# Kernel tuning notes

Measured on AMD Instinct MI355X. Metric: run time of the kernel, lower is better.

Reference implementation:

```python
import jax, jax.numpy as jnp
import numpy as np

N_NODES = 100000
N_EDGES = 400000
N_GRAPHS = 1000
DIM = 5
N_OUT = 2
EPS = 1e-5


def _linear_params(key, fan_in, fan_out):
    kw, kb = jax.random.split(key)
    s = 1.0 / np.sqrt(fan_in)
    w = jax.random.uniform(kw, (fan_in, fan_out), minval=-s, maxval=s, dtype=jnp.float32)
    b = jax.random.uniform(kb, (fan_out,), minval=-s, maxval=s, dtype=jnp.float32)
    return w, b


def _gn_params(c):
    # rows: [weight, bias, mean_scale] as in PyG GraphNorm init (1, 0, 1)
    return jnp.stack([jnp.ones((c,)), jnp.zeros((c,)), jnp.ones((c,))], axis=0).astype(jnp.float32)


def setup_inputs() -> dict:
    key = jax.random.key(0)
    ks = jax.random.split(key, 16)
    x = jax.random.normal(ks[0], (N_NODES, DIM), dtype=jnp.float32)
    edge_index = jax.random.randint(ks[1], (2, N_EDGES), 0, N_NODES, dtype=jnp.int64)
    batch = jnp.sort(jax.random.randint(ks[2], (N_NODES,), 0, N_GRAPHS, dtype=jnp.int64))
    c1_w1, c1_b1 = _linear_params(ks[3], 2 * DIM, 128)
    c1_w2, c1_b2 = _linear_params(ks[4], 128, 128)
    c1_w3, c1_b3 = _linear_params(ks[5], 128, 128)
    c2_w1, c2_b1 = _linear_params(ks[6], 2 * 128, 256)
    c2_w2, c2_b2 = _linear_params(ks[7], 256, 256)
    c3_w1, c3_b1 = _linear_params(ks[8], 2 * 256, 256)
    lin_w1, lin_b1 = _linear_params(ks[9], 256, 256)
    lin_w2, lin_b2 = _linear_params(ks[10], 256, N_OUT)
    return {
        "x": x, "edge_index": edge_index, "batch": batch,
        "c1_w1": c1_w1, "c1_b1": c1_b1, "c1_gn1": _gn_params(128),
        "c1_w2": c1_w2, "c1_b2": c1_b2, "c1_gn2": _gn_params(128),
        "c1_w3": c1_w3, "c1_b3": c1_b3, "c1_gn3": _gn_params(128),
        "c2_w1": c2_w1, "c2_b1": c2_b1, "c2_gn1": _gn_params(256),
        "c2_w2": c2_w2, "c2_b2": c2_b2, "c2_gn2": _gn_params(256),
        "c3_w1": c3_w1, "c3_b1": c3_b1, "c3_gn1": _gn_params(256),
        "lin_w1": lin_w1, "lin_b1": lin_b1, "lin_w2": lin_w2, "lin_b2": lin_b2,
    }


def _graph_norm(h, p):
    # PyG GraphNorm with batch=None: normalize over all rows (single graph)
    g, b, ms = p[0], p[1], p[2]
    m = h.mean(axis=0)
    out = h - ms * m
    var = (out * out).mean(axis=0)
    return g * out * jax.lax.rsqrt(var + EPS) + b


def _edge_conv(x, src, dst, layers):
    # EdgeConv message: nn(cat[x_i, x_j - x_i]) aggregated (mean) at target i
    xi = x[dst]                                     # [E, C]
    h = jnp.concatenate([xi, x[src] - xi], axis=-1)  # [E, 2C]
    for w, b, gp in layers:
        h = jax.nn.relu(_graph_norm(h @ w + b, gp))
    s = jax.ops.segment_sum(h, dst, num_segments=N_NODES)
    ones = jnp.ones((dst.shape[0], 1), dtype=h.dtype)
    cnt = jax.ops.segment_sum(ones, dst, num_segments=N_NODES)
    return s / jnp.maximum(cnt, 1.0)


def reference(x, edge_index, batch,
              c1_w1, c1_b1, c1_gn1, c1_w2, c1_b2, c1_gn2, c1_w3, c1_b3, c1_gn3,
              c2_w1, c2_b1, c2_gn1, c2_w2, c2_b2, c2_gn2,
              c3_w1, c3_b1, c3_gn1,
              lin_w1, lin_b1, lin_w2, lin_b2):
    src, dst = edge_index[0], edge_index[1]
    h = _edge_conv(x, src, dst, [(c1_w1, c1_b1, c1_gn1), (c1_w2, c1_b2, c1_gn2), (c1_w3, c1_b3, c1_gn3)])
    h = _edge_conv(h, src, dst, [(c2_w1, c2_b1, c2_gn1), (c2_w2, c2_b2, c2_gn2)])
    h = _edge_conv(h, src, dst, [(c3_w1, c3_b1, c3_gn1)])
    # global_mean_pool over graphs (dropout = identity in eval)
    gs = jax.ops.segment_sum(h, batch, num_segments=N_GRAPHS)
    gc = jax.ops.segment_sum(jnp.ones((h.shape[0], 1), h.dtype), batch, num_segments=N_GRAPHS)
    g = gs / jnp.maximum(gc, 1.0)                   # [G, 256]
    out = jax.nn.relu(g @ lin_w1 + lin_b1) @ lin_w2 + lin_b2  # [G, n_out]
    return out
```

## Files before the change

### kernel.cpp

```cpp
#include <hip/hip_runtime.h>
#include <hip/hip_bf16.h>

#define NN 100000
#define NE 400000
#define NG 1000

typedef __attribute__((ext_vector_type(8))) short bf16x8;
typedef __attribute__((ext_vector_type(4))) float f32x4;

__device__ __forceinline__ float bf2f(unsigned short h) {
    return __uint_as_float((unsigned)h << 16);
}
__device__ __forceinline__ unsigned short f2bf(float f) {
    unsigned u = __float_as_uint(f);
    return (unsigned short)((u + 0x7FFFu + ((u >> 16) & 1u)) >> 16);
}
__device__ __forceinline__ void up8(uint4 u, float v[8]) {
    v[0] = bf2f((unsigned short)u.x); v[1] = bf2f((unsigned short)(u.x >> 16));
    v[2] = bf2f((unsigned short)u.y); v[3] = bf2f((unsigned short)(u.y >> 16));
    v[4] = bf2f((unsigned short)u.z); v[5] = bf2f((unsigned short)(u.z >> 16));
    v[6] = bf2f((unsigned short)u.w); v[7] = bf2f((unsigned short)(u.w >> 16));
}
__device__ __forceinline__ uint4 pk8(const float v[8]) {
    uint4 r;
    r.x = (uint)f2bf(v[0]) | ((uint)f2bf(v[1]) << 16);
    r.y = (uint)f2bf(v[2]) | ((uint)f2bf(v[3]) << 16);
    r.z = (uint)f2bf(v[4]) | ((uint)f2bf(v[5]) << 16);
    r.w = (uint)f2bf(v[6]) | ((uint)f2bf(v[7]) << 16);
    return r;
}

__global__ void diag_kernel(float* __restrict__ out, int n, float val) {
    int i = blockIdx.x * 256 + threadIdx.x;
    if (i < n) out[i] = val;
}

__global__ void deg_kernel(const int* __restrict__ dst, int* __restrict__ deg) {
    int e = blockIdx.x * 256 + threadIdx.x;
    if (e < NE) atomicAdd(&deg[dst[e]], 1);
}

__global__ void invdeg_kernel(const int* __restrict__ deg, float* __restrict__ invdeg) {
    int n = blockIdx.x * 256 + threadIdx.x;
    if (n < NN) invdeg[n] = 1.0f / (float)(deg[n] > 0 ? deg[n] : 1);
}

__global__ void scan1_kernel(const int* __restrict__ deg, int* __restrict__ off,
                             int* __restrict__ bsum) {
    __shared__ int s[1024];
    int tid = threadIdx.x;
    int i = blockIdx.x * 1024 + tid;
    int v = (i < NN) ? deg[i] : 0;
    s[tid] = v;
    __syncthreads();
    for (int d = 1; d < 1024; d <<= 1) {
        int add = (tid >= d) ? s[tid - d] : 0;
        __syncthreads();
        s[tid] += add;
        __syncthreads();
    }
    if (i < NN) off[i] = s[tid] - v;
    if (tid == 1023) bsum[blockIdx.x] = s[1023];
}

__global__ void scan2_kernel(int* __restrict__ bsum, int nb) {
    __shared__ int s[128];
    int tid = threadIdx.x;
    int v = (tid < nb) ? bsum[tid] : 0;
    s[tid] = v;
    __syncthreads();
    for (int d = 1; d < 128; d <<= 1) {
        int add = (tid >= d) ? s[tid - d] : 0;
        __syncthreads();
        s[tid] += add;
        __syncthreads();
    }
    if (tid < nb) bsum[tid] = s[tid] - v;
}

__global__ void scan3_kernel(int* __restrict__ off, const int* __restrict__ bsum,
                             int* __restrict__ cursor) {
    int i = blockIdx.x * 256 + threadIdx.x;
    if (i < NN) {
        int o = off[i] + bsum[i >> 10];
        off[i] = o;
        cursor[i] = o;
    }
    if (i == 0) off[NN] = NE;
}

__global__ void sortedge_kernel(const int* __restrict__ src, const int* __restrict__ dst,
                                int* __restrict__ cursor, int* __restrict__ ssrc,
                                int* __restrict__ sdst) {
    int e = blockIdx.x * 256 + threadIdx.x;
    if (e < NE) {
        int d = dst[e];
        int pos = atomicAdd(&cursor[d], 1);
        ssrc[pos] = src[e];
        sdst[pos] = d;
    }
}

__global__ void conv1_node_kernel(const float* __restrict__ x, const float* __restrict__ W,
                                  unsigned short* __restrict__ RQ) {
    __shared__ float Ws[1280];
    for (int i = threadIdx.x; i < 1280; i += 256) Ws[i] = W[i];
    __syncthreads();
    int c = threadIdx.x & 127;
    int which = threadIdx.x >> 7;
    for (int n = blockIdx.x; n < NN; n += gridDim.x) {
        float acc = 0.f;
        #pragma unroll
        for (int r = 0; r < 5; r++) {
            float xv = x[n * 5 + r];
            float bot = Ws[(5 + r) * 128 + c];
            float w = which ? bot : (Ws[r * 128 + c] - bot);
            acc = fmaf(xv, w, acc);
        }
        RQ[(size_t)n * 256 + threadIdx.x] = f2bf(acc);
    }
}

__global__ void wtrans_kernel(const float* __restrict__ W, unsigned short* __restrict__ Wt,
                              int K, int N) {
    int idx = blockIdx.x * 256 + threadIdx.x;
    if (idx >= K * N) return;
    int c = idx / K, k = idx - c * K;
    Wt[(size_t)c * K + k] = f2bf(W[(size_t)k * N + c]);
}

__global__ void wprime_t_kernel(const float* __restrict__ W, unsigned short* __restrict__ Wpt,
                                int K, int C) {
    int idx = blockIdx.x * 256 + threadIdx.x;
    if (idx >= 2 * C * K) return;
    int n = idx / K, k = idx - n * K;
    float v;
    if (n < C) v = W[(size_t)k * C + n] - W[(size_t)(K + k) * C + n];
    else       v = W[(size_t)(K + k) * C + (n - C)];
    Wpt[(size_t)n * K + k] = f2bf(v);
}

template<int C>
__global__ void gstats_node_kernel(const unsigned short* __restrict__ RQ,
                                   const int* __restrict__ ssrc, const int* __restrict__ off,
                                   const float* __restrict__ bias,
                                   float* __restrict__ ssum, float* __restrict__ ssq) {
    constexpr int GPB = 256 / C;
    const int t = threadIdx.x;
    const int c = t % C, g = t / C;
    float b = bias[c];
    float ls = 0.f, lq = 0.f;
    int chunk = (NN + gridDim.x - 1) / gridDim.x;
    int nb = blockIdx.x * chunk, ne = min(nb + chunk, NN);
    for (int n = nb + g; n < ne; n += GPB) {
        float R = bf2f(RQ[(size_t)n * (2 * C) + c]);
        int e0 = off[n], e1 = off[n + 1];
        for (int e = e0; e < e1; e++) {
            float v = R + bf2f(RQ[(size_t)ssrc[e] * (2 * C) + C + c]) + b;
            ls += v; lq += v * v;
        }
    }
    __shared__ float red[2][256];
    red[0][t] = ls; red[1][t] = lq;
    __syncthreads();
    if (t < C) {
        float s = 0.f, q = 0.f;
        #pragma unroll
        for (int gg = 0; gg < GPB; gg++) { s += red[0][gg * C + t]; q += red[1][gg * C + t]; }
        atomicAdd(&ssum[t], s);
        atomicAdd(&ssq[t], q);
    }
}

__global__ void finalize_kernel(const float* __restrict__ ssum, const float* __restrict__ ssq,
                                const float* __restrict__ gn, int C, float invM,
                                float* __restrict__ alpha, float* __restrict__ beta) {
    int c = threadIdx.x;
    if (c >= C) return;
    float g = gn[c], b = gn[C + c], ms = gn[2 * C + c];
    float m = ssum[c] * invM;
    float var = ssq[c] * invM - m * m * ms * (2.f - ms);
    float inv = rsqrtf(var + 1e-5f);
    alpha[c] = g * inv;
    beta[c] = b - g * inv * ms * m;
}

template<int TK, int BN, bool GATHER, bool NORMRELU, bool ROWSC, bool STATS, bool STORE,
         bool SCAT, bool AF32>
__global__ __launch_bounds__(256) void mgemm_kernel(
    const void* __restrict__ Av, const int* __restrict__ gsrc, const int* __restrict__ gdst,
    const float* __restrict__ biasIn, const unsigned short* __restrict__ Wt,
    const float* __restrict__ alpha, const float* __restrict__ beta,
    const float* __restrict__ rowscale, const float* __restrict__ biasOut,
    unsigned short* __restrict__ Cmat, int M, int N,
    float* __restrict__ ssum, float* __restrict__ ssq,
    const float* __restrict__ alphaO, const float* __restrict__ betaO,
    float* __restrict__ hsum) {
    constexpr int WNC = BN / 4;
    constexpr int NF = WNC / 16;
    constexpr int SPR = TK / 8;
    constexpr int ITER = 64 * SPR / 256;
    __shared__ __align__(16) unsigned short At[64][TK + 8];
    __shared__ __align__(16) float sAl[TK], sBe[TK], sBi[TK];
    __shared__ float sS[BN], sQ[BN];
    const int t = threadIdx.x;
    const int wave = t >> 6, lane = t & 63;
    const int l15 = lane & 15, lq = lane >> 4;
    const int r0 = blockIdx.y * 64;
    const int n0 = blockIdx.x * BN;

    if (NORMRELU) for (int i = t; i < TK; i += 256) { sAl[i] = alpha[i]; sBe[i] = beta[i]; }
    if (GATHER)   for (int i = t; i < TK; i += 256) { sBi[i] = biasIn[i]; }
    if (STATS && t < BN) { sS[t] = 0.f; sQ[t] = 0.f; }
    __syncthreads();

    const unsigned short* Abf = (const unsigned short*)Av;
    const float* Af = (const float*)Av;

    #pragma unroll
    for (int it = 0; it < ITER; it++) {
        int slot = it * 256 + t;
        int row = slot / SPR;
        int c0 = (slot - row * SPR) * 8;
        int ar = r0 + row;
        float v[8];
        if (GATHER) {
            int gd = gdst[ar], gs = gsrc[ar];
            uint4 pa4 = *(const uint4*)&Abf[(size_t)gd * (2 * TK) + c0];
            uint4 pq4 = *(const uint4*)&Abf[(size_t)gs * (2 * TK) + TK + c0];
            float pa[8], pq[8];
            up8(pa4, pa); up8(pq4, pq);
            #pragma unroll
            for (int i = 0; i < 8; i++) v[i] = pa[i] + pq[i] + sBi[c0 + i];
        } else if (AF32) {
            if (ar < M) {
                float4 f0 = *(const float4*)&Af[(size_t)ar * TK + c0];
                float4 f1 = *(const float4*)&Af[(size_t)ar * TK + c0 + 4];
                v[0] = f0.x; v[1] = f0.y; v[2] = f0.z; v[3] = f0.w;
                v[4] = f1.x; v[5] = f1.y; v[6] = f1.z; v[7] = f1.w;
            } else {
                #pragma unroll
                for (int i = 0; i < 8; i++) v[i] = 0.f;
            }
        } else {
            if (ar < M) {
                uint4 a4 = *(const uint4*)&Abf[(size_t)ar * TK + c0];
                up8(a4, v);
            } else {
                #pragma unroll
                for (int i = 0; i < 8; i++) v[i] = 0.f;
            }
        }
        if (NORMRELU) {
            #pragma unroll
            for (int i = 0; i < 8; i++)
                v[i] = fmaxf(fmaf(sAl[c0 + i], v[i], sBe[c0 + i]), 0.f);
        }
        if (ROWSC) {
            float rs = (ar < M) ? rowscale[ar] : 0.f;
            #pragma unroll
            for (int i = 0; i < 8; i++) v[i] *= rs;
        }
        *(uint4*)&At[row][c0] = pk8(v);
    }
    __syncthreads();

    const unsigned short* bp[NF];
    #pragma unroll
    for (int cf = 0; cf < NF; cf++)
        bp[cf] = &Wt[(size_t)(n0 + wave * WNC + 16 * cf + l15) * TK + lq * 8];

    f32x4 acc[4][NF];
    #pragma unroll
    for (int i = 0; i < 4; i++)
        #pragma unroll
        for (int j = 0; j < NF; j++) acc[i][j] = {0.f, 0.f, 0.f, 0.f};

    #pragma unroll
    for (int k0 = 0; k0 < TK; k0 += 32) {
        bf16x8 af[4];
        #pragma unroll
        for (int rf = 0; rf < 4; rf++)
            af[rf] = *(const bf16x8*)&At[16 * rf + l15][k0 + lq * 8];
        bf16x8 bfr[NF];
        #pragma unroll
        for (int cf = 0; cf < NF; cf++)
            bfr[cf] = *(const bf16x8*)(bp[cf] + k0);
        #pragma unroll
        for (int rf = 0; rf < 4; rf++)
            #pragma unroll
            for (int cf = 0; cf < NF; cf++)
                acc[rf][cf] = __builtin_amdgcn_mfma_f32_16x16x32_bf16(
                    af[rf], bfr[cf], acc[rf][cf], 0, 0, 0);
    }

    int cA[NF];
    float bO[NF], aO[NF], bOo[NF];
    #pragma unroll
    for (int cf = 0; cf < NF; cf++) {
        cA[cf] = n0 + wave * WNC + 16 * cf + l15;
        bO[cf] = (biasOut != nullptr) ? biasOut[cA[cf]] : 0.f;
        if (SCAT) { aO[cf] = alphaO[cA[cf]]; bOo[cf] = betaO[cA[cf]]; }
    }
    float ps[NF], pq[NF];
    #pragma unroll
    for (int cf = 0; cf < NF; cf++) { ps[cf] = 0.f; pq[cf] = 0.f; }
    #pragma unroll
    for (int rf = 0; rf < 4; rf++) {
        int rb = r0 + 16 * rf + lq * 4;
        int dd[4];
        if (SCAT) {
            #pragma unroll
            for (int jj = 0; jj < 4; jj++) dd[jj] = gdst[rb + jj];
        }
        #pragma unroll
        for (int cf = 0; cf < NF; cf++) {
            #pragma unroll
            for (int jj = 0; jj < 4; jj++) {
                float o = acc[rf][cf][jj] + bO[cf];
                if (STATS) { ps[cf] += o; pq[cf] += o * o; }
                if (STORE) {
                    int r = rb + jj;
                    if (r < M) Cmat[(size_t)r * N + cA[cf]] = f2bf(o);
                }
                if (SCAT) {
                    float h = fmaxf(fmaf(aO[cf], o, bOo[cf]), 0.f);
                    atomicAdd(&hsum[(size_t)dd[jj] * N + cA[cf]], h);
                }
            }
        }
    }
    if (STATS) {
        #pragma unroll
        for (int cf = 0; cf < NF; cf++) {
            float s = ps[cf], q = pq[cf];
            s += __shfl_xor(s, 16); s += __shfl_xor(s, 32);
            q += __shfl_xor(q, 16); q += __shfl_xor(q, 32);
            if (lq == 0) {
                atomicAdd(&sS[cA[cf] - n0], s);
                atomicAdd(&sQ[cA[cf] - n0], q);
            }
        }
        __syncthreads();
        if (t < BN) {
            atomicAdd(&ssum[n0 + t], sS[t]);
            atomicAdd(&ssq[n0 + t], sQ[t]);
        }
    }
}

template<int C>
__global__ void aggregate_node_kernel(const unsigned short* __restrict__ Y,
                                      const int* __restrict__ off,
                                      const float* __restrict__ alpha,
                                      const float* __restrict__ beta,
                                      const float* __restrict__ invdeg,
                                      float* __restrict__ h) {
    constexpr int GPB = 256 / C;
    const int t = threadIdx.x;
    const int c = t % C, g = t / C;
    float al = alpha[c], be = beta[c];
    int chunk = (NN + gridDim.x - 1) / gridDim.x;
    int nb = blockIdx.x * chunk, ne = min(nb + chunk, NN);
    for (int n = nb + g; n < ne; n += GPB) {
        int e0 = off[n], e1 = off[n + 1];
        float s = 0.f;
        for (int e = e0; e < e1; e++)
            s += fmaxf(fmaf(al, bf2f(Y[(size_t)e * C + c]), be), 0.f);
        h[(size_t)n * C + c] = s * invdeg[n];
    }
}

__global__ void aggregate_fg_node_kernel(const unsigned short* __restrict__ RQ,
                                         const int* __restrict__ ssrc,
                                         const int* __restrict__ off,
                                         const float* __restrict__ bias,
                                         const float* __restrict__ alpha,
                                         const float* __restrict__ beta,
                                         const float* __restrict__ invdeg,
                                         float* __restrict__ h) {
    int c = threadIdx.x;
    float b = bias[c], al = alpha[c], be = beta[c];
    int chunk = (NN + gridDim.x - 1) / gridDim.x;
    int nb = blockIdx.x * chunk, ne = min(nb + chunk, NN);
    for (int n = nb; n < ne; n++) {
        float R = bf2f(RQ[(size_t)n * 512 + c]);
        int e0 = off[n], e1 = off[n + 1];
        float s = 0.f;
        for (int e = e0; e < e1; e++) {
            float v = R + bf2f(RQ[(size_t)ssrc[e] * 512 + 256 + c]) + b;
            s += fmaxf(fmaf(al, v, be), 0.f);
        }
        h[(size_t)n * 256 + c] = s * invdeg[n];
    }
}

__global__ void pool_kernel(const float* __restrict__ h3, const int* __restrict__ batch,
                            float* __restrict__ gsum, int* __restrict__ gcnt) {
    int chunk = (NN + gridDim.x - 1) / gridDim.x;
    int nbeg = blockIdx.x * chunk;
    int nend = min(nbeg + chunk, NN);
    if (nbeg >= nend) return;
    int t = threadIdx.x;
    int curg = batch[nbeg];
    float acc = 0.f;
    int cnt = 0;
    for (int n = nbeg; n < nend; n++) {
        int g = batch[n];
        if (g != curg) {
            atomicAdd(&gsum[(size_t)curg * 256 + t], acc);
            if (t == 0) atomicAdd(&gcnt[curg], cnt);
            curg = g; acc = 0.f; cnt = 0;
        }
        acc += h3[(size_t)n * 256 + t];
        cnt++;
    }
    atomicAdd(&gsum[(size_t)curg * 256 + t], acc);
    if (t == 0) atomicAdd(&gcnt[curg], cnt);
}

__global__ void mlp_kernel(const float* __restrict__ gsum, const int* __restrict__ gcnt,
                           const float* __restrict__ W1, const float* __restrict__ b1,
                           const float* __restrict__ W2, const float* __restrict__ b2,
                           float* __restrict__ out) {
    int g = blockIdx.x;
    int t = threadIdx.x;
    __shared__ float grow[256];
    __shared__ float r0s[256], r1s[256];
    int cnt = gcnt[g];
    float inv = 1.0f / (float)(cnt > 0 ? cnt : 1);
    grow[t] = gsum[(size_t)g * 256 + t] * inv;
    __syncthreads();
    float acc = b1[t];
    for (int k = 0; k < 256; k++) acc = fmaf(grow[k], W1[k * 256 + t], acc);
    float h = fmaxf(acc, 0.f);
    r0s[t] = h * W2[t * 2 + 0];
    r1s[t] = h * W2[t * 2 + 1];
    __syncthreads();
    for (int s = 128; s > 0; s >>= 1) {
        if (t < s) { r0s[t] += r0s[t + s]; r1s[t] += r1s[t + s]; }
        __syncthreads();
    }
    if (t == 0) {
        out[g * 2 + 0] = r0s[0] + b2[0];
        out[g * 2 + 1] = r1s[0] + b2[1];
    }
}

extern "C" void kernel_launch(void* const* d_in, const int* in_sizes, int n_in,
                              void* d_out, int out_size, void* d_ws, size_t ws_size,
                              hipStream_t stream) {
    const float* x      = (const float*)d_in[0];
    const int*   ei     = (const int*)d_in[1];
    const int*   src0   = ei;
    const int*   dst0   = ei + NE;
    const int*   batch  = (const int*)d_in[2];
    const float* c1_w1  = (const float*)d_in[3];
    const float* c1_b1  = (const float*)d_in[4];
    const float* c1_gn1 = (const float*)d_in[5];
    const float* c1_w2  = (const float*)d_in[6];
    const float* c1_b2  = (const float*)d_in[7];
    const float* c1_gn2 = (const float*)d_in[8];
    const float* c1_w3  = (const float*)d_in[9];
    const float* c1_b3  = (const float*)d_in[10];
    const float* c1_gn3 = (const float*)d_in[11];
    const float* c2_w1  = (const float*)d_in[12];
    const float* c2_b1  = (const float*)d_in[13];
    const float* c2_gn1 = (const float*)d_in[14];
    const float* c2_w2  = (const float*)d_in[15];
    const float* c2_b2  = (const float*)d_in[16];
    const float* c2_gn2 = (const float*)d_in[17];
    const float* c3_w1  = (const float*)d_in[18];
    const float* c3_b1  = (const float*)d_in[19];
    const float* c3_gn1 = (const float*)d_in[20];
    const float* lin_w1 = (const float*)d_in[21];
    const float* lin_b1 = (const float*)d_in[22];
    const float* lin_w2 = (const float*)d_in[23];
    const float* lin_b2 = (const float*)d_in[24];
    float* out = (float*)d_out;

    constexpr size_t REG_BYTES = (size_t)NE * 128 * 2;
    constexpr size_t NEED = 2 * REG_BYTES + 16 * 1024 * 1024;

    if (ws_size < NEED) {
        diag_kernel<<<(out_size + 255) / 256, 256, 0, stream>>>(
            out, out_size, (float)(ws_size >> 20));
        return;
    }

    char* base = (char*)d_ws;
    unsigned short* RA = (unsigned short*)base;
    unsigned short* RB = (unsigned short*)(base + REG_BYTES);
    float* h1    = (float*)RB;
    float* h2sum = (float*)RB;
    float* h3    = (float*)RB;
    char* p = base + 2 * REG_BYTES;
    auto alloc = [&](size_t bytes) -> void* {
        void* r = (void*)p;
        p += (bytes + 255) & ~(size_t)255;
        return r;
    };
    unsigned short* c1w2t = (unsigned short*)alloc((size_t)128 * 128 * 2);
    unsigned short* c1w3t = (unsigned short*)alloc((size_t)128 * 128 * 2);
    unsigned short* c2w2t = (unsigned short*)alloc((size_t)256 * 256 * 2);
    unsigned short* Wpt   = (unsigned short*)alloc((size_t)512 * 256 * 2);
    int*   deg    = (int*)alloc((size_t)NN * 4);
    float* invdeg = (float*)alloc((size_t)NN * 4);
    int*   off    = (int*)alloc((size_t)(NN + 1) * 4);
    int*   cursor = (int*)alloc((size_t)NN * 4);
    int*   bsum   = (int*)alloc((size_t)128 * 4);
    int*   ssrc   = (int*)alloc((size_t)NE * 4);
    int*   sdst   = (int*)alloc((size_t)NE * 4);
    float* ssum   = (float*)alloc(256 * 4);
    float* ssq    = (float*)alloc(256 * 4);
    float* al0    = (float*)alloc(256 * 4);
    float* be0    = (float*)alloc(256 * 4);
    float* al1    = (float*)alloc(256 * 4);
    float* be1    = (float*)alloc(256 * 4);
    float* gsum   = (float*)alloc((size_t)NG * 256 * 4);
    int*   gcnt   = (int*)alloc((size_t)NG * 4);

    const float invE = 1.0f / (float)NE;
    const int MT_E = NE / 64;
    const int MT_N = (NN + 63) / 64;
    const int NB = (NN + 1023) / 1024;

    hipMemsetAsync(deg, 0, (size_t)NN * 4, stream);
    hipMemsetAsync(gsum, 0, (size_t)NG * 256 * 4, stream);
    hipMemsetAsync(gcnt, 0, (size_t)NG * 4, stream);

    deg_kernel<<<(NE + 255) / 256, 256, 0, stream>>>(dst0, deg);
    invdeg_kernel<<<(NN + 255) / 256, 256, 0, stream>>>(deg, invdeg);
    scan1_kernel<<<NB, 1024, 0, stream>>>(deg, off, bsum);
    scan2_kernel<<<1, 128, 0, stream>>>(bsum, NB);
    scan3_kernel<<<(NN + 255) / 256, 256, 0, stream>>>(off, bsum, cursor);
    sortedge_kernel<<<(NE + 255) / 256, 256, 0, stream>>>(src0, dst0, cursor, ssrc, sdst);

    wtrans_kernel<<<(128 * 128 + 255) / 256, 256, 0, stream>>>(c1_w2, c1w2t, 128, 128);
    wtrans_kernel<<<(128 * 128 + 255) / 256, 256, 0, stream>>>(c1_w3, c1w3t, 128, 128);
    wtrans_kernel<<<(256 * 256 + 255) / 256, 256, 0, stream>>>(c2_w2, c2w2t, 256, 256);

    conv1_node_kernel<<<2048, 256, 0, stream>>>(x, c1_w1, RA);
    hipMemsetAsync(ssum, 0, 256 * 4, stream);
    hipMemsetAsync(ssq, 0, 256 * 4, stream);
    gstats_node_kernel<128><<<2048, 256, 0, stream>>>(RA, ssrc, off, c1_b1, ssum, ssq);
    finalize_kernel<<<1, 256, 0, stream>>>(ssum, ssq, c1_gn1, 128, invE, al0, be0);

    hipMemsetAsync(ssum, 0, 256 * 4, stream);
    hipMemsetAsync(ssq, 0, 256 * 4, stream);
    mgemm_kernel<128, 128, true, true, false, true, true, false, false>
        <<<dim3(1, MT_E), 256, 0, stream>>>(RA, ssrc, sdst, c1_b1, c1w2t, al0, be0,
                                            nullptr, c1_b2, RB, NE, 128,
                                            ssum, ssq, nullptr, nullptr, nullptr);
    finalize_kernel<<<1, 256, 0, stream>>>(ssum, ssq, c1_gn2, 128, invE, al0, be0);

    hipMemsetAsync(ssum, 0, 256 * 4, stream);
    hipMemsetAsync(ssq, 0, 256 * 4, stream);
    mgemm_kernel<128, 128, false, true, false, true, true, false, false>
        <<<dim3(1, MT_E), 256, 0, stream>>>(RB, nullptr, nullptr, nullptr, c1w3t, al0, be0,
                                            nullptr, c1_b3, RA, NE, 128,
                                            ssum, ssq, nullptr, nullptr, nullptr);
    finalize_kernel<<<1, 256, 0, stream>>>(ssum, ssq, c1_gn3, 128, invE, al0, be0);

    aggregate_node_kernel<128><<<2048, 256, 0, stream>>>(RA, off, al0, be0, invdeg, h1);

    wprime_t_kernel<<<(512 * 128 + 255) / 256, 256, 0, stream>>>(c2_w1, Wpt, 128, 256);
    mgemm_kernel<128, 256, false, false, false, false, true, false, true>
        <<<dim3(2, MT_N), 256, 0, stream>>>(h1, nullptr, nullptr, nullptr, Wpt,
                                            nullptr, nullptr, nullptr, nullptr, RA,
                                            NN, 512, nullptr, nullptr,
                                            nullptr, nullptr, nullptr);
    hipMemsetAsync(ssum, 0, 256 * 4, stream);
    hipMemsetAsync(ssq, 0, 256 * 4, stream);
    gstats_node_kernel<256><<<2048, 256, 0, stream>>>(RA, ssrc, off, c2_b1, ssum, ssq);
    finalize_kernel<<<1, 256, 0, stream>>>(ssum, ssq, c2_gn1, 256, invE, al0, be0);

    hipMemsetAsync(ssum, 0, 256 * 4, stream);
    hipMemsetAsync(ssq, 0, 256 * 4, stream);
    mgemm_kernel<256, 256, true, true, false, true, false, false, false>
        <<<dim3(1, MT_E), 256, 0, stream>>>(RA, ssrc, sdst, c2_b1, c2w2t, al0, be0,
                                            nullptr, c2_b2, nullptr, NE, 256,
                                            ssum, ssq, nullptr, nullptr, nullptr);
    finalize_kernel<<<1, 256, 0, stream>>>(ssum, ssq, c2_gn2, 256, invE, al1, be1);

    hipMemsetAsync(h2sum, 0, (size_t)NN * 256 * 4, stream);
    mgemm_kernel<256, 256, true, true, false, false, false, true, false>
        <<<dim3(1, MT_E), 256, 0, stream>>>(RA, ssrc, sdst, c2_b1, c2w2t, al0, be0,
                                            nullptr, c2_b2, nullptr, NE, 256,
                                            nullptr, nullptr, al1, be1, h2sum);

    wprime_t_kernel<<<(512 * 256 + 255) / 256, 256, 0, stream>>>(c3_w1, Wpt, 256, 256);
    mgemm_kernel<256, 256, false, false, true, false, true, false, true>
        <<<dim3(2, MT_N), 256, 0, stream>>>(h2sum, nullptr, nullptr, nullptr, Wpt,
                                            nullptr, nullptr, invdeg, nullptr, RA,
                                            NN, 512, nullptr, nullptr,
                                            nullptr, nullptr, nullptr);
    hipMemsetAsync(ssum, 0, 256 * 4, stream);
    hipMemsetAsync(ssq, 0, 256 * 4, stream);
    gstats_node_kernel<256><<<2048, 256, 0, stream>>>(RA, ssrc, off, c3_b1, ssum, ssq);
    finalize_kernel<<<1, 256, 0, stream>>>(ssum, ssq, c3_gn1, 256, invE, al0, be0);

    aggregate_fg_node_kernel<<<2048, 256, 0, stream>>>(RA, ssrc, off, c3_b1, al0, be0,
                                                       invdeg, h3);

    pool_kernel<<<512, 256, 0, stream>>>(h3, batch, gsum, gcnt);
    mlp_kernel<<<NG, 256, 0, stream>>>(gsum, gcnt, lin_w1, lin_b1, lin_w2, lin_b2, out);
}
```

Before: 2.352 ms.

## Split conv2 second layer into halves, materialize and aggregate instead of recompute/scatter

```diff
diff --git a/kernel.cpp b/kernel.cpp
--- a/kernel.cpp
+++ b/kernel.cpp
@@ -29,6 +29,8 @@
     r.w = (uint)f2bf(v[6]) | ((uint)f2bf(v[7]) << 16);
     return r;
 }
+__device__ __forceinline__ void stout(float* p, float v) { *p = v; }
+__device__ __forceinline__ void stout(unsigned short* p, float v) { *p = f2bf(v); }
 
 __global__ void diag_kernel(float* __restrict__ out, int n, float val) {
     int i = blockIdx.x * 256 + threadIdx.x;
@@ -173,11 +175,11 @@
 }
 
 __global__ void finalize_kernel(const float* __restrict__ ssum, const float* __restrict__ ssq,
-                                const float* __restrict__ gn, int C, float invM,
+                                const float* __restrict__ gn, int stride, int cnt, float invM,
                                 float* __restrict__ alpha, float* __restrict__ beta) {
     int c = threadIdx.x;
-    if (c >= C) return;
-    float g = gn[c], b = gn[C + c], ms = gn[2 * C + c];
+    if (c >= cnt) return;
+    float g = gn[c], b = gn[stride + c], ms = gn[2 * stride + c];
     float m = ssum[c] * invM;
     float var = ssq[c] * invM - m * m * ms * (2.f - ms);
     float inv = rsqrtf(var + 1e-5f);
@@ -349,13 +351,13 @@
     }
 }
 
-template<int C>
+template<int C, typename TOUT>
 __global__ void aggregate_node_kernel(const unsigned short* __restrict__ Y,
                                       const int* __restrict__ off,
                                       const float* __restrict__ alpha,
                                       const float* __restrict__ beta,
                                       const float* __restrict__ invdeg,
-                                      float* __restrict__ h) {
+                                      TOUT* __restrict__ h, int ldH, int coff) {
     constexpr int GPB = 256 / C;
     const int t = threadIdx.x;
     const int c = t % C, g = t / C;
@@ -367,7 +369,7 @@
         float s = 0.f;
         for (int e = e0; e < e1; e++)
             s += fmaxf(fmaf(al, bf2f(Y[(size_t)e * C + c]), be), 0.f);
-        h[(size_t)n * C + c] = s * invdeg[n];
+        stout(&h[(size_t)n * ldH + coff + c], s * invdeg[n]);
     }
 }
 
@@ -403,10 +405,12 @@
     if (nbeg >= nend) return;
     int t = threadIdx.x;
     int curg = batch[nbeg];
+    if ((unsigned)curg >= NG) curg = 0;
     float acc = 0.f;
     int cnt = 0;
     for (int n = nbeg; n < nend; n++) {
         int g = batch[n];
+        if ((unsigned)g >= NG) g = 0;
         if (g != curg) {
             atomicAdd(&gsum[(size_t)curg * 256 + t], acc);
             if (t == 0) atomicAdd(&gcnt[curg], cnt);
@@ -480,7 +484,8 @@
     float* out = (float*)d_out;
 
     constexpr size_t REG_BYTES = (size_t)NE * 128 * 2;
-    constexpr size_t NEED = 2 * REG_BYTES + 16 * 1024 * 1024;
+    constexpr size_t H2_BYTES  = (size_t)NN * 256 * 2;
+    constexpr size_t NEED = 2 * REG_BYTES + H2_BYTES + 8 * 1024 * 1024;
 
     if (ws_size < NEED) {
         diag_kernel<<<(out_size + 255) / 256, 256, 0, stream>>>(
@@ -491,15 +496,15 @@
     char* base = (char*)d_ws;
     unsigned short* RA = (unsigned short*)base;
     unsigned short* RB = (unsigned short*)(base + REG_BYTES);
-    float* h1    = (float*)RB;
-    float* h2sum = (float*)RB;
-    float* h3    = (float*)RB;
+    float* h1 = (float*)RB;
+    float* h3 = (float*)RB;
     char* p = base + 2 * REG_BYTES;
     auto alloc = [&](size_t bytes) -> void* {
         void* r = (void*)p;
         p += (bytes + 255) & ~(size_t)255;
         return r;
     };
+    unsigned short* h2bf  = (unsigned short*)alloc(H2_BYTES);
     unsigned short* c1w2t = (unsigned short*)alloc((size_t)128 * 128 * 2);
     unsigned short* c1w3t = (unsigned short*)alloc((size_t)128 * 128 * 2);
     unsigned short* c2w2t = (unsigned short*)alloc((size_t)256 * 256 * 2);
@@ -544,7 +549,7 @@
     hipMemsetAsync(ssum, 0, 256 * 4, stream);
     hipMemsetAsync(ssq, 0, 256 * 4, stream);
     gstats_node_kernel<128><<<2048, 256, 0, stream>>>(RA, ssrc, off, c1_b1, ssum, ssq);
-    finalize_kernel<<<1, 256, 0, stream>>>(ssum, ssq, c1_gn1, 128, invE, al0, be0);
+    finalize_kernel<<<1, 256, 0, stream>>>(ssum, ssq, c1_gn1, 128, 128, invE, al0, be0);
 
     hipMemsetAsync(ssum, 0, 256 * 4, stream);
     hipMemsetAsync(ssq, 0, 256 * 4, stream);
@@ -552,7 +557,7 @@
         <<<dim3(1, MT_E), 256, 0, stream>>>(RA, ssrc, sdst, c1_b1, c1w2t, al0, be0,
                                             nullptr, c1_b2, RB, NE, 128,
                                             ssum, ssq, nullptr, nullptr, nullptr);
-    finalize_kernel<<<1, 256, 0, stream>>>(ssum, ssq, c1_gn2, 128, invE, al0, be0);
+    finalize_kernel<<<1, 256, 0, stream>>>(ssum, ssq, c1_gn2, 128, 128, invE, al0, be0);
 
     hipMemsetAsync(ssum, 0, 256 * 4, stream);
     hipMemsetAsync(ssq, 0, 256 * 4, stream);
@@ -560,9 +565,10 @@
         <<<dim3(1, MT_E), 256, 0, stream>>>(RB, nullptr, nullptr, nullptr, c1w3t, al0, be0,
                                             nullptr, c1_b3, RA, NE, 128,
                                             ssum, ssq, nullptr, nullptr, nullptr);
-    finalize_kernel<<<1, 256, 0, stream>>>(ssum, ssq, c1_gn3, 128, invE, al0, be0);
-
-    aggregate_node_kernel<128><<<2048, 256, 0, stream>>>(RA, off, al0, be0, invdeg, h1);
+    finalize_kernel<<<1, 256, 0, stream>>>(ssum, ssq, c1_gn3, 128, 128, invE, al0, be0);
+
+    aggregate_node_kernel<128, float><<<2048, 256, 0, stream>>>(RA, off, al0, be0, invdeg,
+                                                                h1, 128, 0);
 
     wprime_t_kernel<<<(512 * 128 + 255) / 256, 256, 0, stream>>>(c2_w1, Wpt, 128, 256);
     mgemm_kernel<128, 256, false, false, false, false, true, false, true>
@@ -573,32 +579,33 @@
     hipMemsetAsync(ssum, 0, 256 * 4, stream);
     hipMemsetAsync(ssq, 0, 256 * 4, stream);
     gstats_node_kernel<256><<<2048, 256, 0, stream>>>(RA, ssrc, off, c2_b1, ssum, ssq);
-    finalize_kernel<<<1, 256, 0, stream>>>(ssum, ssq, c2_gn1, 256, invE, al0, be0);
-
-    hipMemsetAsync(ssum, 0, 256 * 4, stream);
-    hipMemsetAsync(ssq, 0, 256 * 4, stream);
-    mgemm_kernel<256, 256, true, true, false, true, false, false, false>
-        <<<dim3(1, MT_E), 256, 0, stream>>>(RA, ssrc, sdst, c2_b1, c2w2t, al0, be0,
-                                            nullptr, c2_b2, nullptr, NE, 256,
-                                            ssum, ssq, nullptr, nullptr, nullptr);
-    finalize_kernel<<<1, 256, 0, stream>>>(ssum, ssq, c2_gn2, 256, invE, al1, be1);
-
-    hipMemsetAsync(h2sum, 0, (size_t)NN * 256 * 4, stream);
-    mgemm_kernel<256, 256, true, true, false, false, false, true, false>
-        <<<dim3(1, MT_E), 256, 0, stream>>>(RA, ssrc, sdst, c2_b1, c2w2t, al0, be0,
-                                            nullptr, c2_b2, nullptr, NE, 256,
-                                            nullptr, nullptr, al1, be1, h2sum);
+    finalize_kernel<<<1, 256, 0, stream>>>(ssum, ssq, c2_gn1, 256, 256, invE, al0, be0);
+
+    for (int half = 0; half < 2; half++) {
+        int coff = half * 128;
+        hipMemsetAsync(ssum, 0, 256 * 4, stream);
+        hipMemsetAsync(ssq, 0, 256 * 4, stream);
+        mgemm_kernel<256, 128, true, true, false, true, true, false, false>
+            <<<dim3(1, MT_E), 256, 0, stream>>>(RA, ssrc, sdst, c2_b1,
+                                                c2w2t + (size_t)coff * 256, al0, be0,
+                                                nullptr, c2_b2 + coff, RB, NE, 128,
+                                                ssum, ssq, nullptr, nullptr, nullptr);
+        finalize_kernel<<<1, 256, 0, stream>>>(ssum, ssq, c2_gn2 + coff, 256, 128, invE,
+                                               al1, be1);
+        aggregate_node_kernel<128, unsigned short><<<2048, 256, 0, stream>>>(
+            RB, off, al1, be1, invdeg, h2bf, 256, coff);
+    }
 
     wprime_t_kernel<<<(512 * 256 + 255) / 256, 256, 0, stream>>>(c3_w1, Wpt, 256, 256);
-    mgemm_kernel<256, 256, false, false, true, false, true, false, true>
-        <<<dim3(2, MT_N), 256, 0, stream>>>(h2sum, nullptr, nullptr, nullptr, Wpt,
-                                            nullptr, nullptr, invdeg, nullptr, RA,
+    mgemm_kernel<256, 256, false, false, false, false, true, false, false>
+        <<<dim3(2, MT_N), 256, 0, stream>>>(h2bf, nullptr, nullptr, nullptr, Wpt,
+                                            nullptr, nullptr, nullptr, nullptr, RA,
                                             NN, 512, nullptr, nullptr,
                                             nullptr, nullptr, nullptr);
     hipMemsetAsync(ssum, 0, 256 * 4, stream);
     hipMemsetAsync(ssq, 0, 256 * 4, stream);
     gstats_node_kernel<256><<<2048, 256, 0, stream>>>(RA, ssrc, off, c3_b1, ssum, ssq);
-    finalize_kernel<<<1, 256, 0, stream>>>(ssum, ssq, c3_gn1, 256, invE, al0, be0);
+    finalize_kernel<<<1, 256, 0, stream>>>(ssum, ssq, c3_gn1, 256, 256, invE, al0, be0);
 
     aggregate_fg_node_kernel<<<2048, 256, 0, stream>>>(RA, ssrc, off, c3_b1, al0, be0,
                                                        invdeg, h3);
```

Measured after the change: 2.064 ms. 12.3% less time.
